# Kernel optimization log

Measured on AMD Instinct MI355X. Metric: run time of the kernel, lower is better.

## Reference

```python
import jax, jax.numpy as jnp
import numpy as np

H, W = 512, 512
N = H * W
NCLS = 4
D_BI, D_SP = 5, 2
THETA_ALPHA, THETA_BETA, THETA_GAMMA = 80.0, 0.0625, 3.0
BI_COMPAT, SP_COMPAT, COMPATIBILITY = 10.0, 3.0, -1.0
NUM_ITER = 10


def _build_lattice(feats):
    """Permutohedral lattice precompute (numpy, integer index construction).
    feats: [N, d]. Returns os [N,d+1] int32 (1-based), ws [N,d+1] float32,
    bn [d+1, M, 2] int32 (0 = missing neighbor), M."""
    feats = np.asarray(feats, np.float64)
    n, d = feats.shape
    inv_std = np.sqrt(2.0 / 3.0) * (d + 1)
    scale = inv_std / np.sqrt((np.arange(d) + 1.0) * (np.arange(d) + 2.0))
    cf = feats * scale
    # embedding matrix E: elevated = cf @ E.T lies on the hyperplane sum=0
    E = np.zeros((d + 1, d))
    E[0, :] = 1.0
    for j in range(1, d + 1):
        E[j, j:] = 1.0
        E[j, j - 1] = -j
    elevated = cf @ E.T  # [n, d+1]
    greedy = (np.rint(elevated / (d + 1)) * (d + 1)).astype(np.int64)
    diff = elevated - greedy
    idx = np.arange(d + 1)
    upper = idx[None, :] > idx[:, None]
    lower = idx[None, :] < idx[:, None]
    di = diff[:, :, None]
    dj = diff[:, None, :]
    rank = (((dj > di) & upper) | ((dj >= di) & lower)).sum(-1)
    rank = rank + greedy.sum(1, keepdims=True) // (d + 1)
    low = rank < 0
    rank = rank + np.where(low, d + 1, 0)
    greedy = greedy + np.where(low, d + 1, 0)
    high = rank > d
    rank = rank - np.where(high, d + 1, 0)
    greedy = greedy - np.where(high, d + 1, 0)
    # barycentric weights
    bary = np.zeros((n, d + 2))
    v = (elevated - greedy) / (d + 1)
    rows = np.repeat(np.arange(n), d + 1)
    np.add.at(bary, (rows, (d - rank).ravel()), v.ravel())
    np.add.at(bary, (rows, (d + 1 - rank).ravel()), -v.ravel())
    bary[:, 0] += 1.0 + bary[:, d + 1]
    ws = bary[:, : d + 1].astype(np.float32)
    # simplex vertex keys (first d coords; last is implied by zero-sum)
    keys = np.empty((n, d + 1, d), np.int64)
    for r in range(d + 1):
        keys[:, r, :] = (greedy + r - (d + 1) * (rank > d - r))[:, :d]
    flat = keys.reshape(-1, d)
    lo = flat.min(0) - (d + 1)
    hi = flat.max(0) + (d + 1)
    strides = np.cumprod(np.concatenate([[1], (hi - lo + 1)[:-1]]))
    coords = (flat - lo) @ strides
    uniq, first, inv = np.unique(coords, return_index=True, return_inverse=True)
    M = int(len(uniq))
    os_ = (inv.reshape(n, d + 1) + 1).astype(np.int32)
    ukeys = flat[first]
    bn = np.zeros((d + 1, M, 2), np.int32)
    for j in range(d + 1):
        n1 = ukeys - 1
        n2 = ukeys + 1
        if j < d:
            n1[:, j] = ukeys[:, j] + d
            n2[:, j] = ukeys[:, j] - d
        for t, nk in enumerate((n1, n2)):
            c = (nk - lo) @ strides
            pos = np.clip(np.searchsorted(uniq, c), 0, M - 1)
            bn[j, :, t] = np.where(uniq[pos] == c, pos + 1, 0)
    return os_, ws, bn, M


def setup_inputs() -> dict:
    key = jax.random.key(0)
    k1, k2 = jax.random.split(key)
    image = jax.random.uniform(k1, (H, W, 7), dtype=jnp.float32)
    unary = jax.random.normal(k2, (H, W, NCLS), dtype=jnp.float32)
    img = np.asarray(image)
    yy, xx = np.mgrid[0:H, 0:W].astype(np.float64)
    bifeat = np.concatenate(
        [(xx / THETA_ALPHA)[..., None], (yy / THETA_ALPHA)[..., None],
         img[..., :3] / THETA_BETA], axis=-1).reshape(N, D_BI)
    spfeat = np.stack([xx / THETA_GAMMA, yy / THETA_GAMMA], -1).reshape(N, D_SP)
    os_b, ws_b, bn_b, M_b = _build_lattice(bifeat)
    os_s, ws_s, bn_s, M_s = _build_lattice(spfeat)
    return {
        "unary": unary,
        "ws_bilateral": jnp.asarray(ws_b), "os_bilateral": jnp.asarray(os_b),
        "blur_neighbors_bilateral": jnp.asarray(bn_b), "M_bilateral": M_b,
        "ws_spatial": jnp.asarray(ws_s), "os_spatial": jnp.asarray(os_s),
        "blur_neighbors_spatial": jnp.asarray(bn_s), "M_spatial": M_s,
    }


def _perm_filter(values, os_, ws, bn, M, alpha):
    # values: [N, C]; splat -> blur -> slice
    d1 = os_.shape[1]
    C = values.shape[1]
    table = jnp.zeros((M + 1, C), values.dtype)  # row 0 = dummy (missing)
    table = table.at[os_.reshape(-1)].add(
        (values[:, None, :] * ws[:, :, None]).reshape(-1, C))
    for j in range(d1):  # [0.5, 1, 0.5] blur along each lattice axis
        table = table.at[1:].add(0.5 * (table[bn[j, :, 0]] + table[bn[j, :, 1]]))
    return alpha * jnp.einsum("nrc,nr->nc", table[os_], ws)


def _mean_field(unary, ws_b, os_b, bn_b, M_b, ws_s, os_s, bn_s, M_s):
    C = unary.shape[-1]
    u = unary.reshape(N, C)
    alpha_b = 1.0 / (1.0 + 2.0 ** (-D_BI))
    alpha_s = 1.0 / (1.0 + 2.0 ** (-D_SP))
    ones = jnp.ones((N, 1), u.dtype)
    inv_nb = 1.0 / (_perm_filter(ones, os_b, ws_b, bn_b, M_b, alpha_b) + 1e-20)
    inv_ns = 1.0 / (_perm_filter(ones, os_s, ws_s, bn_s, M_s, alpha_s) + 1e-20)
    Q = jax.nn.softmax(-u, axis=-1)
    for _ in range(NUM_ITER):
        msg = (BI_COMPAT * _perm_filter(Q, os_b, ws_b, bn_b, M_b, alpha_b) * inv_nb
               + SP_COMPAT * _perm_filter(Q, os_s, ws_s, bn_s, M_s, alpha_s) * inv_ns)
        Q = jax.nn.softmax(-u - COMPATIBILITY * msg, axis=-1)
    return Q.reshape(H, W, C)


def reference(unary, ws_bilateral, os_bilateral, blur_neighbors_bilateral, M_bilateral,
              ws_spatial, os_spatial, blur_neighbors_spatial, M_spatial):
    # Returns the refined marginals Q [H, W, NCLS]; the module's MAP output is
    # jnp.argmax(Q, -1) (kept soft here so fwd/bwd share one output).
    return _mean_field(unary, ws_bilateral, os_bilateral, blur_neighbors_bilateral,
                       M_bilateral, ws_spatial, os_spatial, blur_neighbors_spatial,
                       M_spatial)
```

## Files before the change

### kernel.cpp

```cpp
#include <hip/hip_runtime.h>

#define NPIX (512 * 512)
#define BLK 256

#define SCAN_T 256
#define SCAN_E 8
#define SCAN_CHUNK (SCAN_T * SCAN_E)

#define TOTB (NPIX * 6)
#define TOTS (NPIX * 3)
#define TOTE (NPIX * 9)

typedef _Float16 h4 __attribute__((ext_vector_type(4)));

constexpr float ALPHA_B = 32.0f / 33.0f;
constexpr float ALPHA_S = 0.8f;
constexpr float BI_COMPAT = 10.0f;
constexpr float SP_COMPAT = 3.0f;

__device__ __forceinline__ unsigned pack_ent(int n, float w) {
    float wc = fminf(fmaxf(w, 0.f), 1.f);
    unsigned iw = (unsigned)(wc * 16383.f + 0.5f);
    return (iw << 18) | (unsigned)n;
}
__device__ __forceinline__ int ent_pix(unsigned e) { return (int)(e & 0x3FFFFu); }
__device__ __forceinline__ float ent_w(unsigned e) {
    return (float)(e >> 18) * (1.0f / 16383.0f);
}

__device__ __forceinline__ float4 f4zero() { return make_float4(0.f, 0.f, 0.f, 0.f); }
__device__ __forceinline__ h4 h4zero() {
    h4 z; z.x = (_Float16)0.f; z.y = (_Float16)0.f; z.z = (_Float16)0.f; z.w = (_Float16)0.f;
    return z;
}

__global__ void k_softmax_init(const float4* __restrict__ u, float4* __restrict__ Q) {
    int n = blockIdx.x * BLK + threadIdx.x;
    if (n >= NPIX) return;
    float4 uu = u[n];
    float l0 = -uu.x, l1 = -uu.y, l2 = -uu.z, l3 = -uu.w;
    float m = fmaxf(fmaxf(l0, l1), fmaxf(l2, l3));
    float e0 = expf(l0 - m), e1 = expf(l1 - m), e2 = expf(l2 - m), e3 = expf(l3 - m);
    float inv = 1.0f / (e0 + e1 + e2 + e3);
    Q[n] = make_float4(e0 * inv, e1 * inv, e2 * inv, e3 * inv);
}

__global__ void k_count_link_softmax(const int* __restrict__ osb, const int* __restrict__ oss,
                                     int* __restrict__ cnt, int* __restrict__ head,
                                     int* __restrict__ next,
                                     const float4* __restrict__ u, float4* __restrict__ Q,
                                     int Vb) {
    int n = blockIdx.x * BLK + threadIdx.x;
    if (n >= NPIX) return;
    float4 uu = u[n];
    float l0 = -uu.x, l1 = -uu.y, l2 = -uu.z, l3 = -uu.w;
    float m = fmaxf(fmaxf(l0, l1), fmaxf(l2, l3));
    float e0 = expf(l0 - m), e1 = expf(l1 - m), e2 = expf(l2 - m), e3 = expf(l3 - m);
    float inv = 1.0f / (e0 + e1 + e2 + e3);
    Q[n] = make_float4(e0 * inv, e1 * inv, e2 * inv, e3 * inv);
#pragma unroll
    for (int r = 0; r < 6; r++) {
        int o = osb[n * 6 + r];
        int e = n * 6 + r;
        atomicAdd(&cnt[o], 1);
        next[e] = atomicExch(&head[o], e);
    }
#pragma unroll
    for (int r = 0; r < 3; r++) {
        int o = Vb + oss[n * 3 + r];
        int e = TOTB + n * 3 + r;
        atomicAdd(&cnt[o], 1);
        next[e] = atomicExch(&head[o], e);
    }
}

__global__ void k_chunk_sum(const int* __restrict__ counts, int V, int* __restrict__ csum) {
    __shared__ int lds[SCAN_T];
    int base = blockIdx.x * SCAN_CHUNK;
    int s = 0;
#pragma unroll
    for (int j = 0; j < SCAN_E; j++) {
        int idx = base + threadIdx.x * SCAN_E + j;
        if (idx < V) s += counts[idx];
    }
    lds[threadIdx.x] = s;
    __syncthreads();
    for (int off = SCAN_T / 2; off > 0; off >>= 1) {
        if ((int)threadIdx.x < off) lds[threadIdx.x] += lds[threadIdx.x + off];
        __syncthreads();
    }
    if (threadIdx.x == 0) csum[blockIdx.x] = lds[0];
}

__global__ void k_scan_csum(int* __restrict__ csum, int nchunks) {
    __shared__ int lds[SCAN_T];
    int carry = 0;
    for (int base = 0; base < nchunks; base += SCAN_T) {
        int idx = base + threadIdx.x;
        int v = (idx < nchunks) ? csum[idx] : 0;
        lds[threadIdx.x] = v;
        __syncthreads();
        for (int off = 1; off < SCAN_T; off <<= 1) {
            int t = ((int)threadIdx.x >= off) ? lds[threadIdx.x - off] : 0;
            __syncthreads();
            lds[threadIdx.x] += t;
            __syncthreads();
        }
        int incl = lds[threadIdx.x];
        int tile_total = lds[SCAN_T - 1];
        if (idx < nchunks) csum[idx] = incl - v + carry;
        carry += tile_total;
        __syncthreads();
    }
}

__global__ void k_chunk_scan(const int* __restrict__ counts, int V,
                             const int* __restrict__ csum, int* __restrict__ start) {
    __shared__ int lds[SCAN_T];
    int base = blockIdx.x * SCAN_CHUNK;
    int local[SCAN_E];
    int s = 0;
#pragma unroll
    for (int j = 0; j < SCAN_E; j++) {
        int idx = base + threadIdx.x * SCAN_E + j;
        int c = (idx < V) ? counts[idx] : 0;
        local[j] = c;
        s += c;
    }
    lds[threadIdx.x] = s;
    __syncthreads();
    for (int off = 1; off < SCAN_T; off <<= 1) {
        int t = ((int)threadIdx.x >= off) ? lds[threadIdx.x - off] : 0;
        __syncthreads();
        lds[threadIdx.x] += t;
        __syncthreads();
    }
    int excl = lds[threadIdx.x] - s + csum[blockIdx.x];
#pragma unroll
    for (int j = 0; j < SCAN_E; j++) {
        int idx = base + threadIdx.x * SCAN_E + j;
        if (idx < V) start[idx] = excl;
        excl += local[j];
    }
}

__global__ void k_compact(const int* __restrict__ head, const int* __restrict__ next,
                          const int* __restrict__ start,
                          const float* __restrict__ wsb, const float* __restrict__ wss,
                          unsigned* __restrict__ ent, int V, int Vb) {
    int o = blockIdx.x * BLK + threadIdx.x;
    if (o >= V) return;
    int p = start[o];
    int e = head[o];
    if (o < Vb) {
        while (e >= 0) {
            unsigned n = (unsigned)e / 6u;
            ent[p++] = pack_ent((int)n, wsb[e]);
            e = next[e];
        }
    } else {
        while (e >= 0) {
            int ee = e - TOTB;
            unsigned n = (unsigned)ee / 3u;
            ent[p++] = pack_ent((int)n, wss[ee]);
            e = next[e];
        }
    }
}

__global__ void k_gather1_both(const unsigned* __restrict__ ent, const int* __restrict__ start,
                               int V, int Vb,
                               float* __restrict__ nB, float* __restrict__ nS) {
    int i = blockIdx.x * BLK + threadIdx.x;
    if (i >= V) return;
    int s = start[i];
    int e = (i + 1 < V) ? start[i + 1] : TOTE;
    float acc = 0.f;
    for (int k = s; k < e; k++) acc += ent_w(ent[k]);
    if (i < Vb) nB[i] = acc;
    else nS[i - Vb] = acc;
}

__global__ void k_gather4h_both(const unsigned* __restrict__ ent, const int* __restrict__ start,
                                int V, int Vb,
                                h4* __restrict__ tB, h4* __restrict__ tS,
                                const float4* __restrict__ Q) {
    int i = blockIdx.x * BLK + threadIdx.x;
    if (i >= V) return;
    int s = start[i];
    int e = (i + 1 < V) ? start[i + 1] : TOTE;
    float ax = 0.f, ay = 0.f, az = 0.f, aw = 0.f;
    for (int k = s; k < e; k++) {
        unsigned en = ent[k];
        float w = ent_w(en);
        float4 q = Q[ent_pix(en)];
        ax += w * q.x; ay += w * q.y; az += w * q.z; aw += w * q.w;
    }
    h4 h;
    h.x = (_Float16)ax; h.y = (_Float16)ay; h.z = (_Float16)az; h.w = (_Float16)aw;
    if (i < Vb) tB[i] = h;
    else tS[i - Vb] = h;
}

__global__ void k_blur1(const float* __restrict__ in, float* __restrict__ out,
                        const int* __restrict__ bn, int M) {
    int i = blockIdx.x * BLK + threadIdx.x;
    if (i > M) return;
    if (i == 0) { out[0] = 0.f; return; }
    int n1 = bn[(size_t)(i - 1) * 2 + 0];
    int n2 = bn[(size_t)(i - 1) * 2 + 1];
    out[i] = in[i] + 0.5f * (in[n1] + in[n2]);
}

__global__ void k_blur1_both(const float* __restrict__ inB, float* __restrict__ outB,
                             const int* __restrict__ bnB, int Mb,
                             const float* __restrict__ inS, float* __restrict__ outS,
                             const int* __restrict__ bnS, int Ms) {
    int i = blockIdx.x * BLK + threadIdx.x;
    const float* in; float* out; const int* bn; int M, idx;
    if (i <= Mb) { in = inB; out = outB; bn = bnB; M = Mb; idx = i; }
    else {
        idx = i - (Mb + 1);
        if (idx > Ms) return;
        in = inS; out = outS; bn = bnS; M = Ms;
    }
    if (idx == 0) { out[0] = 0.f; return; }
    int n1 = bn[(size_t)(idx - 1) * 2 + 0];
    int n2 = bn[(size_t)(idx - 1) * 2 + 1];
    out[idx] = in[idx] + 0.5f * (in[n1] + in[n2]);
}

__global__ void k_blur4h(const h4* __restrict__ in, h4* __restrict__ out,
                         const int* __restrict__ bn, int M) {
    int i = blockIdx.x * BLK + threadIdx.x;
    if (i > M) return;
    if (i == 0) { out[0] = h4zero(); return; }
    int n1 = bn[(size_t)(i - 1) * 2 + 0];
    int n2 = bn[(size_t)(i - 1) * 2 + 1];
    h4 a = in[i], b = in[n1], c = in[n2];
    h4 o;
    o.x = (_Float16)((float)a.x + 0.5f * ((float)b.x + (float)c.x));
    o.y = (_Float16)((float)a.y + 0.5f * ((float)b.y + (float)c.y));
    o.z = (_Float16)((float)a.z + 0.5f * ((float)b.z + (float)c.z));
    o.w = (_Float16)((float)a.w + 0.5f * ((float)b.w + (float)c.w));
    out[i] = o;
}

__global__ void k_blur4h_both(const h4* __restrict__ inB, h4* __restrict__ outB,
                              const int* __restrict__ bnB, int Mb,
                              const h4* __restrict__ inS, h4* __restrict__ outS,
                              const int* __restrict__ bnS, int Ms) {
    int i = blockIdx.x * BLK + threadIdx.x;
    const h4* in; h4* out; const int* bn; int M, idx;
    if (i <= Mb) { in = inB; out = outB; bn = bnB; M = Mb; idx = i; }
    else {
        idx = i - (Mb + 1);
        if (idx > Ms) return;
        in = inS; out = outS; bn = bnS; M = Ms;
    }
    if (idx == 0) { out[0] = h4zero(); return; }
    int n1 = bn[(size_t)(idx - 1) * 2 + 0];
    int n2 = bn[(size_t)(idx - 1) * 2 + 1];
    h4 a = in[idx], b = in[n1], c = in[n2];
    h4 o;
    o.x = (_Float16)((float)a.x + 0.5f * ((float)b.x + (float)c.x));
    o.y = (_Float16)((float)a.y + 0.5f * ((float)b.y + (float)c.y));
    o.z = (_Float16)((float)a.z + 0.5f * ((float)b.z + (float)c.z));
    o.w = (_Float16)((float)a.w + 0.5f * ((float)b.w + (float)c.w));
    out[idx] = o;
}

__global__ void k_norm_prescale(const float* __restrict__ nTb, const float* __restrict__ wsb,
                                const int* __restrict__ osb,
                                const float* __restrict__ nTs, const float* __restrict__ wss,
                                const int* __restrict__ oss,
                                float* __restrict__ wsbp, float* __restrict__ wssp) {
    int n = blockIdx.x * BLK + threadIdx.x;
    if (n >= NPIX) return;
    float sb = 0.f;
#pragma unroll
    for (int r = 0; r < 6; r++) sb += wsb[n * 6 + r] * nTb[osb[n * 6 + r]];
    float cb = BI_COMPAT * ALPHA_B / (ALPHA_B * sb + 1e-20f);
#pragma unroll
    for (int r = 0; r < 6; r++) wsbp[n * 6 + r] = wsb[n * 6 + r] * cb;
    float ss = 0.f;
#pragma unroll
    for (int r = 0; r < 3; r++) ss += wss[n * 3 + r] * nTs[oss[n * 3 + r]];
    float cs = SP_COMPAT * ALPHA_S / (ALPHA_S * ss + 1e-20f);
#pragma unroll
    for (int r = 0; r < 3; r++) wssp[n * 3 + r] = wss[n * 3 + r] * cs;
}

__global__ void k_slice_combine_h(const float4* __restrict__ u,
                                  const h4* __restrict__ tb, const float* __restrict__ wsbp,
                                  const int* __restrict__ osb,
                                  const h4* __restrict__ ts, const float* __restrict__ wssp,
                                  const int* __restrict__ oss,
                                  float4* __restrict__ Qout) {
    int n = blockIdx.x * BLK + threadIdx.x;
    if (n >= NPIX) return;
    float4 uu = u[n];
    float l0 = -uu.x, l1 = -uu.y, l2 = -uu.z, l3 = -uu.w;
#pragma unroll
    for (int r = 0; r < 6; r++) {
        float w = wsbp[n * 6 + r];
        h4 t = tb[osb[n * 6 + r]];
        l0 += w * (float)t.x; l1 += w * (float)t.y; l2 += w * (float)t.z; l3 += w * (float)t.w;
    }
#pragma unroll
    for (int r = 0; r < 3; r++) {
        float w = wssp[n * 3 + r];
        h4 t = ts[oss[n * 3 + r]];
        l0 += w * (float)t.x; l1 += w * (float)t.y; l2 += w * (float)t.z; l3 += w * (float)t.w;
    }
    float m = fmaxf(fmaxf(l0, l1), fmaxf(l2, l3));
    float e0 = expf(l0 - m), e1 = expf(l1 - m), e2 = expf(l2 - m), e3 = expf(l3 - m);
    float inv = 1.0f / (e0 + e1 + e2 + e3);
    Qout[n] = make_float4(e0 * inv, e1 * inv, e2 * inv, e3 * inv);
}

template <int D1>
__global__ void k_splat1(const float* __restrict__ ws, const int* __restrict__ os,
                         float* __restrict__ table) {
    int n = blockIdx.x * BLK + threadIdx.x;
    if (n >= NPIX) return;
#pragma unroll
    for (int r = 0; r < D1; r++) atomicAdd(&table[os[n * D1 + r]], ws[n * D1 + r]);
}

template <int D1>
__global__ void k_splat4(const float4* __restrict__ Q, const float* __restrict__ ws,
                         const int* __restrict__ os, float* __restrict__ table) {
    int n = blockIdx.x * BLK + threadIdx.x;
    if (n >= NPIX) return;
    float4 q = Q[n];
#pragma unroll
    for (int r = 0; r < D1; r++) {
        float w = ws[n * D1 + r];
        int o = os[n * D1 + r];
        float* t = table + 4 * (size_t)o;
        atomicAdd(t + 0, q.x * w);
        atomicAdd(t + 1, q.y * w);
        atomicAdd(t + 2, q.z * w);
        atomicAdd(t + 3, q.w * w);
    }
}

__global__ void k_blur4(const float4* __restrict__ in, float4* __restrict__ out,
                        const int* __restrict__ bn, int M) {
    int i = blockIdx.x * BLK + threadIdx.x;
    if (i > M) return;
    if (i == 0) { out[0] = f4zero(); return; }
    int n1 = bn[(size_t)(i - 1) * 2 + 0];
    int n2 = bn[(size_t)(i - 1) * 2 + 1];
    float4 a = in[i], b = in[n1], c = in[n2];
    out[i] = make_float4(a.x + 0.5f * (b.x + c.x), a.y + 0.5f * (b.y + c.y),
                         a.z + 0.5f * (b.z + c.z), a.w + 0.5f * (b.w + c.w));
}

template <int D1>
__global__ void k_norm_slice(const float* __restrict__ table, const float* __restrict__ ws,
                             const int* __restrict__ os, float alpha,
                             float* __restrict__ inv_out) {
    int n = blockIdx.x * BLK + threadIdx.x;
    if (n >= NPIX) return;
    float s = 0.f;
#pragma unroll
    for (int r = 0; r < D1; r++) s += ws[n * D1 + r] * table[os[n * D1 + r]];
    inv_out[n] = 1.0f / (alpha * s + 1e-20f);
}

__global__ void k_slice_combine(const float4* __restrict__ u,
                                const float4* __restrict__ tb, const float* __restrict__ wsb,
                                const int* __restrict__ osb,
                                const float4* __restrict__ ts, const float* __restrict__ wss,
                                const int* __restrict__ oss,
                                const float* __restrict__ inv_nb,
                                const float* __restrict__ inv_ns,
                                float4* __restrict__ Qout) {
    int n = blockIdx.x * BLK + threadIdx.x;
    if (n >= NPIX) return;
    float4 ab = f4zero();
#pragma unroll
    for (int r = 0; r < 6; r++) {
        float w = wsb[n * 6 + r];
        float4 t = tb[osb[n * 6 + r]];
        ab.x += w * t.x; ab.y += w * t.y; ab.z += w * t.z; ab.w += w * t.w;
    }
    float4 as = f4zero();
#pragma unroll
    for (int r = 0; r < 3; r++) {
        float w = wss[n * 3 + r];
        float4 t = ts[oss[n * 3 + r]];
        as.x += w * t.x; as.y += w * t.y; as.z += w * t.z; as.w += w * t.w;
    }
    float cb = BI_COMPAT * ALPHA_B * inv_nb[n];
    float cs = SP_COMPAT * ALPHA_S * inv_ns[n];
    float4 uu = u[n];
    float l0 = -uu.x + cb * ab.x + cs * as.x;
    float l1 = -uu.y + cb * ab.y + cs * as.y;
    float l2 = -uu.z + cb * ab.z + cs * as.z;
    float l3 = -uu.w + cb * ab.w + cs * as.w;
    float m = fmaxf(fmaxf(l0, l1), fmaxf(l2, l3));
    float e0 = expf(l0 - m), e1 = expf(l1 - m), e2 = expf(l2 - m), e3 = expf(l3 - m);
    float inv = 1.0f / (e0 + e1 + e2 + e3);
    Qout[n] = make_float4(e0 * inv, e1 * inv, e2 * inv, e3 * inv);
}

extern "C" void kernel_launch(void* const* d_in, const int* in_sizes, int n_in,
                              void* d_out, int out_size, void* d_ws, size_t ws_size,
                              hipStream_t stream) {
    const float* unary = (const float*)d_in[0];
    const float* wsb   = (const float*)d_in[1];
    const int*   osb   = (const int*)d_in[2];
    const int*   bnb   = (const int*)d_in[3];
    const float* wss   = (const float*)d_in[5];
    const int*   oss   = (const int*)d_in[6];
    const int*   bns   = (const int*)d_in[7];
    const int Mb = in_sizes[3] / 12;
    const int Ms = in_sizes[7] / 6;
    const int Vb = Mb + 1, Vs = Ms + 1;
    const int V = Vb + Vs;

    float* Q = (float*)d_out;

    char* p = (char*)d_ws;
    auto alloc = [&](size_t nbytes) -> void* {
        void* r = (void*)p;
        p += (nbytes + 15) & ~(size_t)15;
        return r;
    };
    h4*   tAb  = (h4*)alloc((size_t)Vb * 8);
    h4*   tBb  = (h4*)alloc((size_t)Vb * 8);
    h4*   tAs  = (h4*)alloc((size_t)Vs * 8);
    h4*   tBs  = (h4*)alloc((size_t)Vs * 8);
    float* nAb = (float*)alloc((size_t)Vb * 4);
    float* nBb = (float*)alloc((size_t)Vb * 4);
    float* nAs = (float*)alloc((size_t)Vs * 4);
    float* nBs = (float*)alloc((size_t)Vs * 4);
    float* wsbp = (float*)alloc((size_t)NPIX * 6 * 4);
    float* wssp = (float*)alloc((size_t)NPIX * 3 * 4);
    int*   next = (int*)wsbp;
    int*  start = (int*)alloc((size_t)V * 4);
    int*  cnt   = (int*)alloc((size_t)V * 4);
    int*  head  = (int*)alloc((size_t)V * 4);
    unsigned* ent = (unsigned*)alloc((size_t)TOTE * 4);
    int*  csum  = (int*)alloc(8192 * 4);
    size_t need = (size_t)(p - (char*)d_ws);
    bool use_gather = need <= ws_size;

    dim3 blk(BLK);
    dim3 gN((NPIX + BLK - 1) / BLK);
    dim3 gVb((Vb + BLK - 1) / BLK);
    dim3 gV((V + BLK - 1) / BLK);

    if (use_gather) {
        int nch = (V + SCAN_CHUNK - 1) / SCAN_CHUNK;
        hipMemsetAsync(cnt, 0, (size_t)V * 4, stream);
        hipMemsetAsync(head, 0xFF, (size_t)V * 4, stream);
        k_count_link_softmax<<<gN, blk, 0, stream>>>(osb, oss, cnt, head, next,
                                                     (const float4*)unary, (float4*)Q, Vb);
        k_chunk_sum<<<dim3(nch), dim3(SCAN_T), 0, stream>>>(cnt, V, csum);
        k_scan_csum<<<dim3(1), dim3(SCAN_T), 0, stream>>>(csum, nch);
        k_chunk_scan<<<dim3(nch), dim3(SCAN_T), 0, stream>>>(cnt, V, csum, start);
        k_compact<<<gV, blk, 0, stream>>>(head, next, start, wsb, wss, ent, V, Vb);

        k_gather1_both<<<gV, blk, 0, stream>>>(ent, start, V, Vb, nAb, nAs);
        {
            float* a = nAb; float* b = nBb;
            float* as_ = nAs; float* bs_ = nBs;
            for (int j = 0; j < 3; j++) {
                k_blur1_both<<<gV, blk, 0, stream>>>(a, b, bnb + (size_t)j * Mb * 2, Mb,
                                                     as_, bs_, bns + (size_t)j * Ms * 2, Ms);
                float* t = a; a = b; b = t;
                t = as_; as_ = bs_; bs_ = t;
            }
            for (int j = 3; j < 6; j++) {
                k_blur1<<<gVb, blk, 0, stream>>>(a, b, bnb + (size_t)j * Mb * 2, Mb);
                float* t = a; a = b; b = t;
            }
            k_norm_prescale<<<gN, blk, 0, stream>>>(a, wsb, osb, as_, wss, oss, wsbp, wssp);
        }

        for (int it = 0; it < 10; it++) {
            k_gather4h_both<<<gV, blk, 0, stream>>>(ent, start, V, Vb, tAb, tAs,
                                                    (const float4*)Q);
            h4* a = tAb; h4* b = tBb;
            h4* as_ = tAs; h4* bs_ = tBs;
            for (int j = 0; j < 3; j++) {
                k_blur4h_both<<<gV, blk, 0, stream>>>(a, b, bnb + (size_t)j * Mb * 2, Mb,
                                                      as_, bs_, bns + (size_t)j * Ms * 2, Ms);
                h4* t = a; a = b; b = t;
                t = as_; as_ = bs_; bs_ = t;
            }
            for (int j = 3; j < 6; j++) {
                k_blur4h<<<gVb, blk, 0, stream>>>(a, b, bnb + (size_t)j * Mb * 2, Mb);
                h4* t = a; a = b; b = t;
            }
            k_slice_combine_h<<<gN, blk, 0, stream>>>((const float4*)unary,
                                                      a, wsbp, osb, as_, wssp, oss,
                                                      (float4*)Q);
        }
    } else {
        char* q = (char*)d_ws;
        auto alloc2 = [&](size_t nbytes) -> void* {
            void* r = (void*)q;
            q += (nbytes + 15) & ~(size_t)15;
            return r;
        };
        float* fAb = (float*)alloc2((size_t)Vb * 4 * sizeof(float));
        float* fBb = (float*)alloc2((size_t)Vb * 4 * sizeof(float));
        float* fAs = (float*)alloc2((size_t)Vs * 4 * sizeof(float));
        float* fBs = (float*)alloc2((size_t)Vs * 4 * sizeof(float));
        float* inv_nb = (float*)alloc2(NPIX * sizeof(float));
        float* inv_ns = (float*)alloc2(NPIX * sizeof(float));
        dim3 gMb((Mb + 1 + BLK - 1) / BLK);
        dim3 gMs((Ms + 1 + BLK - 1) / BLK);

        hipMemsetAsync(fAb, 0, (size_t)Vb * sizeof(float), stream);
        k_splat1<6><<<gN, blk, 0, stream>>>(wsb, osb, fAb);
        {
            float* a = fAb; float* b = fBb;
            for (int j = 0; j < 6; j++) {
                k_blur1<<<gMb, blk, 0, stream>>>(a, b, bnb + (size_t)j * Mb * 2, Mb);
                float* t = a; a = b; b = t;
            }
            k_norm_slice<6><<<gN, blk, 0, stream>>>(a, wsb, osb, ALPHA_B, inv_nb);
        }
        hipMemsetAsync(fAs, 0, (size_t)Vs * sizeof(float), stream);
        k_splat1<3><<<gN, blk, 0, stream>>>(wss, oss, fAs);
        {
            float* a = fAs; float* b = fBs;
            for (int j = 0; j < 3; j++) {
                k_blur1<<<gMs, blk, 0, stream>>>(a, b, bns + (size_t)j * Ms * 2, Ms);
                float* t = a; a = b; b = t;
            }
            k_norm_slice<3><<<gN, blk, 0, stream>>>(a, wss, oss, ALPHA_S, inv_ns);
        }
        k_softmax_init<<<gN, blk, 0, stream>>>((const float4*)unary, (float4*)Q);
        for (int it = 0; it < 10; it++) {
            hipMemsetAsync(fAb, 0, (size_t)Vb * 4 * sizeof(float), stream);
            k_splat4<6><<<gN, blk, 0, stream>>>((const float4*)Q, wsb, osb, fAb);
            float* a = fAb; float* b = fBb;
            for (int j = 0; j < 6; j++) {
                k_blur4<<<gMb, blk, 0, stream>>>((const float4*)a, (float4*)b,
                                                 bnb + (size_t)j * Mb * 2, Mb);
                float* t = a; a = b; b = t;
            }
            float* finb = a;
            hipMemsetAsync(fAs, 0, (size_t)Vs * 4 * sizeof(float), stream);
            k_splat4<3><<<gN, blk, 0, stream>>>((const float4*)Q, wss, oss, fAs);
            float* as_ = fAs; float* bs_ = fBs;
            for (int j = 0; j < 3; j++) {
                k_blur4<<<gMs, blk, 0, stream>>>((const float4*)as_, (float4*)bs_,
                                                 bns + (size_t)j * Ms * 2, Ms);
                float* t = as_; as_ = bs_; bs_ = t;
            }
            float* fins = as_;
            k_slice_combine<<<gN, blk, 0, stream>>>((const float4*)unary,
                                                    (const float4*)finb, wsb, osb,
                                                    (const float4*)fins, wss, oss,
                                                    inv_nb, inv_ns, (float4*)Q);
        }
    }
}
```

Baseline: 1.075 ms.

## Replace count/scan/compact pipeline with block-local scan and atomic cursor

```diff
diff --git a/kernel.cpp b/kernel.cpp
--- a/kernel.cpp
+++ b/kernel.cpp
@@ -2,10 +2,6 @@
 
 #define NPIX (512 * 512)
 #define BLK 256
-
-#define SCAN_T 256
-#define SCAN_E 8
-#define SCAN_CHUNK (SCAN_T * SCAN_E)
 
 #define TOTB (NPIX * 6)
 #define TOTS (NPIX * 3)
@@ -45,11 +41,10 @@
     Q[n] = make_float4(e0 * inv, e1 * inv, e2 * inv, e3 * inv);
 }
 
-__global__ void k_count_link_softmax(const int* __restrict__ osb, const int* __restrict__ oss,
-                                     int* __restrict__ cnt, int* __restrict__ head,
-                                     int* __restrict__ next,
-                                     const float4* __restrict__ u, float4* __restrict__ Q,
-                                     int Vb) {
+__global__ void k_link_softmax(const int* __restrict__ osb, const int* __restrict__ oss,
+                               int* __restrict__ head, int* __restrict__ next,
+                               const float4* __restrict__ u, float4* __restrict__ Q,
+                               int Vb) {
     int n = blockIdx.x * BLK + threadIdx.x;
     if (n >= NPIX) return;
     float4 uu = u[n];
@@ -62,133 +57,72 @@
     for (int r = 0; r < 6; r++) {
         int o = osb[n * 6 + r];
         int e = n * 6 + r;
-        atomicAdd(&cnt[o], 1);
         next[e] = atomicExch(&head[o], e);
     }
 #pragma unroll
     for (int r = 0; r < 3; r++) {
         int o = Vb + oss[n * 3 + r];
         int e = TOTB + n * 3 + r;
-        atomicAdd(&cnt[o], 1);
         next[e] = atomicExch(&head[o], e);
     }
 }
 
-__global__ void k_chunk_sum(const int* __restrict__ counts, int V, int* __restrict__ csum) {
-    __shared__ int lds[SCAN_T];
-    int base = blockIdx.x * SCAN_CHUNK;
-    int s = 0;
-#pragma unroll
-    for (int j = 0; j < SCAN_E; j++) {
-        int idx = base + threadIdx.x * SCAN_E + j;
-        if (idx < V) s += counts[idx];
-    }
-    lds[threadIdx.x] = s;
+__global__ void k_compact(const int* __restrict__ head, const int* __restrict__ next,
+                          const float* __restrict__ wsb, const float* __restrict__ wss,
+                          unsigned* __restrict__ ent, int* __restrict__ start,
+                          int* __restrict__ endv,
+                          float* __restrict__ nB, float* __restrict__ nS,
+                          int* __restrict__ cursor, int V, int Vb) {
+    __shared__ int lds[BLK];
+    __shared__ int sbase;
+    int o = blockIdx.x * BLK + threadIdx.x;
+    bool valid = o < V;
+    int h = valid ? head[o] : -1;
+    int len = 0;
+    for (int e = h; e >= 0; e = next[e]) len++;
+    lds[threadIdx.x] = len;
     __syncthreads();
-    for (int off = SCAN_T / 2; off > 0; off >>= 1) {
-        if ((int)threadIdx.x < off) lds[threadIdx.x] += lds[threadIdx.x + off];
-        __syncthreads();
-    }
-    if (threadIdx.x == 0) csum[blockIdx.x] = lds[0];
-}
-
-__global__ void k_scan_csum(int* __restrict__ csum, int nchunks) {
-    __shared__ int lds[SCAN_T];
-    int carry = 0;
-    for (int base = 0; base < nchunks; base += SCAN_T) {
-        int idx = base + threadIdx.x;
-        int v = (idx < nchunks) ? csum[idx] : 0;
-        lds[threadIdx.x] = v;
-        __syncthreads();
-        for (int off = 1; off < SCAN_T; off <<= 1) {
-            int t = ((int)threadIdx.x >= off) ? lds[threadIdx.x - off] : 0;
-            __syncthreads();
-            lds[threadIdx.x] += t;
-            __syncthreads();
-        }
-        int incl = lds[threadIdx.x];
-        int tile_total = lds[SCAN_T - 1];
-        if (idx < nchunks) csum[idx] = incl - v + carry;
-        carry += tile_total;
-        __syncthreads();
-    }
-}
-
-__global__ void k_chunk_scan(const int* __restrict__ counts, int V,
-                             const int* __restrict__ csum, int* __restrict__ start) {
-    __shared__ int lds[SCAN_T];
-    int base = blockIdx.x * SCAN_CHUNK;
-    int local[SCAN_E];
-    int s = 0;
-#pragma unroll
-    for (int j = 0; j < SCAN_E; j++) {
-        int idx = base + threadIdx.x * SCAN_E + j;
-        int c = (idx < V) ? counts[idx] : 0;
-        local[j] = c;
-        s += c;
-    }
-    lds[threadIdx.x] = s;
-    __syncthreads();
-    for (int off = 1; off < SCAN_T; off <<= 1) {
+    for (int off = 1; off < BLK; off <<= 1) {
         int t = ((int)threadIdx.x >= off) ? lds[threadIdx.x - off] : 0;
         __syncthreads();
         lds[threadIdx.x] += t;
         __syncthreads();
     }
-    int excl = lds[threadIdx.x] - s + csum[blockIdx.x];
-#pragma unroll
-    for (int j = 0; j < SCAN_E; j++) {
-        int idx = base + threadIdx.x * SCAN_E + j;
-        if (idx < V) start[idx] = excl;
-        excl += local[j];
-    }
-}
-
-__global__ void k_compact(const int* __restrict__ head, const int* __restrict__ next,
-                          const int* __restrict__ start,
-                          const float* __restrict__ wsb, const float* __restrict__ wss,
-                          unsigned* __restrict__ ent, int V, int Vb) {
-    int o = blockIdx.x * BLK + threadIdx.x;
-    if (o >= V) return;
-    int p = start[o];
-    int e = head[o];
+    int incl = lds[threadIdx.x];
+    if (threadIdx.x == BLK - 1) sbase = atomicAdd(cursor, incl);
+    __syncthreads();
+    if (!valid) return;
+    int pos = sbase + incl - len;
+    start[o] = pos;
+    endv[o] = pos + len;
+    float acc = 0.f;
     if (o < Vb) {
-        while (e >= 0) {
+        for (int e = h; e >= 0; e = next[e]) {
             unsigned n = (unsigned)e / 6u;
-            ent[p++] = pack_ent((int)n, wsb[e]);
-            e = next[e];
-        }
+            unsigned pe = pack_ent((int)n, wsb[e]);
+            acc += ent_w(pe);
+            ent[pos++] = pe;
+        }
+        nB[o] = acc;
     } else {
-        while (e >= 0) {
+        for (int e = h; e >= 0; e = next[e]) {
             int ee = e - TOTB;
-            unsigned n = (unsigned)ee / 3u;
-            ent[p++] = pack_ent((int)n, wss[ee]);
-            e = next[e];
-        }
-    }
-}
-
-__global__ void k_gather1_both(const unsigned* __restrict__ ent, const int* __restrict__ start,
-                               int V, int Vb,
-                               float* __restrict__ nB, float* __restrict__ nS) {
+            unsigned pe = pack_ent(ee / 3, wss[ee]);
+            acc += ent_w(pe);
+            ent[pos++] = pe;
+        }
+        nS[o - Vb] = acc;
+    }
+}
+
+__global__ void k_gather4h_both(const unsigned* __restrict__ ent, const int* __restrict__ start,
+                                const int* __restrict__ endv, int V, int Vb,
+                                h4* __restrict__ tB, h4* __restrict__ tS,
+                                const float4* __restrict__ Q) {
     int i = blockIdx.x * BLK + threadIdx.x;
     if (i >= V) return;
     int s = start[i];
-    int e = (i + 1 < V) ? start[i + 1] : TOTE;
-    float acc = 0.f;
-    for (int k = s; k < e; k++) acc += ent_w(ent[k]);
-    if (i < Vb) nB[i] = acc;
-    else nS[i - Vb] = acc;
-}
-
-__global__ void k_gather4h_both(const unsigned* __restrict__ ent, const int* __restrict__ start,
-                                int V, int Vb,
-                                h4* __restrict__ tB, h4* __restrict__ tS,
-                                const float4* __restrict__ Q) {
-    int i = blockIdx.x * BLK + threadIdx.x;
-    if (i >= V) return;
-    int s = start[i];
-    int e = (i + 1 < V) ? start[i + 1] : TOTE;
+    int e = endv[i];
     float ax = 0.f, ay = 0.f, az = 0.f, aw = 0.f;
     for (int k = s; k < e; k++) {
         unsigned en = ent[k];
@@ -442,10 +376,10 @@
     float* wssp = (float*)alloc((size_t)NPIX * 3 * 4);
     int*   next = (int*)wsbp;
     int*  start = (int*)alloc((size_t)V * 4);
-    int*  cnt   = (int*)alloc((size_t)V * 4);
+    int*  endv  = (int*)alloc((size_t)V * 4);
     int*  head  = (int*)alloc((size_t)V * 4);
     unsigned* ent = (unsigned*)alloc((size_t)TOTE * 4);
-    int*  csum  = (int*)alloc(8192 * 4);
+    int*  cursor = (int*)alloc(16);
     size_t need = (size_t)(p - (char*)d_ws);
     bool use_gather = need <= ws_size;
 
@@ -455,17 +389,13 @@
     dim3 gV((V + BLK - 1) / BLK);
 
     if (use_gather) {
-        int nch = (V + SCAN_CHUNK - 1) / SCAN_CHUNK;
-        hipMemsetAsync(cnt, 0, (size_t)V * 4, stream);
         hipMemsetAsync(head, 0xFF, (size_t)V * 4, stream);
-        k_count_link_softmax<<<gN, blk, 0, stream>>>(osb, oss, cnt, head, next,
-                                                     (const float4*)unary, (float4*)Q, Vb);
-        k_chunk_sum<<<dim3(nch), dim3(SCAN_T), 0, stream>>>(cnt, V, csum);
-        k_scan_csum<<<dim3(1), dim3(SCAN_T), 0, stream>>>(csum, nch);
-        k_chunk_scan<<<dim3(nch), dim3(SCAN_T), 0, stream>>>(cnt, V, csum, start);
-        k_compact<<<gV, blk, 0, stream>>>(head, next, start, wsb, wss, ent, V, Vb);
-
-        k_gather1_both<<<gV, blk, 0, stream>>>(ent, start, V, Vb, nAb, nAs);
+        hipMemsetAsync(cursor, 0, 16, stream);
+        k_link_softmax<<<gN, blk, 0, stream>>>(osb, oss, head, next,
+                                               (const float4*)unary, (float4*)Q, Vb);
+        k_compact<<<gV, blk, 0, stream>>>(head, next, wsb, wss, ent, start, endv,
+                                          nAb, nAs, cursor, V, Vb);
+
         {
             float* a = nAb; float* b = nBb;
             float* as_ = nAs; float* bs_ = nBs;
@@ -483,7 +413,7 @@
         }
 
         for (int it = 0; it < 10; it++) {
-            k_gather4h_both<<<gV, blk, 0, stream>>>(ent, start, V, Vb, tAb, tAs,
+            k_gather4h_both<<<gV, blk, 0, stream>>>(ent, start, endv, V, Vb, tAb, tAs,
                                                     (const float4*)Q);
             h4* a = tAb; h4* b = tBb;
             h4* as_ = tAs; h4* bs_ = tBs;
```

Result: faster. 952.4 us (-11.4%).
